# Optimization experiments

Hardware: AMD Instinct MI355X
Metric: run time of the kernel (lower is better)

## Reference

```python
import jax, jax.numpy as jnp
import numpy as np

NEG_INF = -1.0e10  # matches -10000000000.0 in the original


def setup_inputs() -> dict:
    key0 = jax.random.key(0)
    kq, kk, kv = jax.random.split(key0, 3)
    b, t, n, n_kv, d = 1, 2048, 32, 8, 128
    query = jax.random.normal(kq, (b, t, n, d), dtype=jnp.float32)
    key = jax.random.normal(kk, (b, t, n_kv, d), dtype=jnp.float32)
    value = jax.random.normal(kv, (b, t, n_kv, d), dtype=jnp.float32)
    return {"query": query, "key": key, "value": value}


def reference(query, key, value):
    """PagedAttentionOp prefill path: paged_dot_product_attention_with_max_and_sum.

    Returns (attn, local_max, local_sums) exactly as the flax module does.
    """
    b, t, n, d = query.shape
    _, s, n_kv, _ = key.shape
    g = n // n_kv  # query heads per KV head (GQA group size)
    q = jnp.reshape(query, (b, t, n_kv, g, d))
    # [b, n_kv, g, t, s]
    attn_weights = jnp.einsum("btkgd,bskd->bkgts", q, key)
    causal_mask = jnp.triu(jnp.ones((t, s), dtype=bool), k=1)[None, None, None]
    masked = jnp.where(causal_mask, NEG_INF, attn_weights)
    local_max = jnp.max(masked, axis=-1, keepdims=True)          # [b,k,g,t,1]
    local_exps = jnp.exp(masked - local_max)
    local_sums = jnp.sum(local_exps, axis=-1, keepdims=True)     # [b,k,g,t,1]
    attn = jnp.einsum("bkgts,bskd->btkgd", local_exps, value)
    attn = jnp.reshape(attn, (b, t, n, d))
    # move the t axis to position 1 then flatten (k,g) -> n
    local_max = jnp.reshape(jnp.moveaxis(local_max, -2, 1), (b, t, n, 1))
    local_sums = jnp.reshape(jnp.moveaxis(local_sums, -2, 1), (b, t, n, 1))
    return attn, local_max, local_sums
```

## Files before the change

### kernel.cpp

```cpp
#include <hip/hip_runtime.h>
#include <hip/hip_bf16.h>

#define TT  2048
#define NH  32
#define NKV 8
#define DD  128
#define KVB 64
#define THR 8.0f

typedef __attribute__((ext_vector_type(8)))  short  short8;
typedef __attribute__((ext_vector_type(4)))  float  f32x4;
typedef __attribute__((ext_vector_type(16))) float  f32x16;
typedef unsigned int u32;
typedef __attribute__((ext_vector_type(4)))  u32    u32x4;

static __device__ __forceinline__ short f2bf(float x) {
  __bf16 b = (__bf16)x;
  return __builtin_bit_cast(short, b);
}
static __device__ __forceinline__ short8 cvt8(f32x4 a, f32x4 b) {
  short8 r;
  r[0]=f2bf(a[0]); r[1]=f2bf(a[1]); r[2]=f2bf(a[2]); r[3]=f2bf(a[3]);
  r[4]=f2bf(b[0]); r[5]=f2bf(b[1]); r[6]=f2bf(b[2]); r[7]=f2bf(b[3]);
  return r;
}
static __device__ __forceinline__ u32 pk2(float lo, float hi) {
  const u32 a = (u32)(unsigned short)f2bf(lo);
  const u32 b = (u32)(unsigned short)f2bf(hi);
  return a | (b << 16);
}
static __device__ __forceinline__ void gload_lds16(const short* g, short* l) {
  __builtin_amdgcn_global_load_lds(
      (const __attribute__((address_space(1))) u32*)g,
      (__attribute__((address_space(3))) u32*)l, 16, 0, 0);
}

__global__ __launch_bounds__(256) void preconv(
    const float* __restrict__ K, const float* __restrict__ V,
    short* __restrict__ Kbf, short* __restrict__ Vtbf)
{
  const int t = threadIdx.x;
  if (blockIdx.x >= 256) {
    const int b  = blockIdx.x - 256;
    const int rr = (b << 6) + (t >> 2);
    const int q  = t & 3;
    const int j = rr >> 3, kvh = rr & 7;
    const float* src = K + (size_t)rr * DD + q * 32;
    short* dst = Kbf + ((size_t)kvh * TT + j) * DD + q * 32;
#pragma unroll
    for (int i = 0; i < 4; ++i) {
      f32x4 a  = *reinterpret_cast<const f32x4*>(src + i * 8);
      f32x4 bb = *reinterpret_cast<const f32x4*>(src + i * 8 + 4);
      *reinterpret_cast<short8*>(dst + i * 8) = cvt8(a, bb);
    }
  } else {
    const int kvh = blockIdx.x >> 5, jt = blockIdx.x & 31;
    __shared__ short Vl[64][136];
    const int jl = t >> 2, q = t & 3;
    const float* src = V + ((size_t)(jt * 64 + jl) * NKV + kvh) * DD + q * 32;
#pragma unroll
    for (int i = 0; i < 4; ++i) {
      f32x4 a  = *reinterpret_cast<const f32x4*>(src + i * 8);
      f32x4 bb = *reinterpret_cast<const f32x4*>(src + i * 8 + 4);
      *reinterpret_cast<short8*>(&Vl[jl][q * 32 + i * 8]) = cvt8(a, bb);
    }
    __syncthreads();
    const int d = t >> 1, jh = t & 1;
    short8 o[4];
#pragma unroll
    for (int k = 0; k < 4; ++k)
#pragma unroll
      for (int i = 0; i < 8; ++i)
        o[k][i] = Vl[jh * 32 + k * 8 + i][d];
    short* dst = Vtbf + ((size_t)kvh * DD + d) * TT + jt * 64 + jh * 32;
#pragma unroll
    for (int k = 0; k < 4; ++k)
      *reinterpret_cast<short8*>(dst + k * 8) = o[k];
  }
}

__global__ __launch_bounds__(512, 2) void attn_fwd(
    const float* __restrict__ Q, const short* __restrict__ Kbf,
    const short* __restrict__ Vtbf, float* __restrict__ O,
    float* __restrict__ Mo, float* __restrict__ Lo)
{
  __shared__ __align__(16) short smem[2*KVB*DD + 2*DD*KVB];
  __shared__ float sx[3][2][4][32];

  short (*Kb)[KVB][DD] = reinterpret_cast<short(*)[KVB][DD]>(&smem[0]);
  short (*Vt)[DD][KVB] = reinterpret_cast<short(*)[DD][KVB]>(&smem[2*KVB*DD]);

  const int bid  = blockIdx.x;
  const int kvh  = bid & (NKV - 1);
  const int q32  = 63 - (bid >> 3);
  const int wv   = threadIdx.x >> 6;
  const int headq= wv & 3;
  const int kh   = wv >> 2;
  const int lane = threadIdx.x & 63;
  const int l31  = lane & 31;
  const int hiK  = lane >> 5;
  const int l7   = lane & 7;
  const int head = kvh * 4 + headq;
  const int qbase = q32 * 32;
  const int q    = qbase + l31;

  const int krow0 = 8 * wv + (lane >> 4);
  const int koff0 = krow0 * DD + ((lane & 15) ^ (krow0 & 7)) * 8;
  const int krow1 = krow0 + 4;
  const int koff1 = krow1 * DD + ((lane & 15) ^ (krow1 & 7)) * 8;
  const int vrow0 = 16 * wv + (lane >> 3);
  const int voff0 = vrow0 * TT + ((lane & 7) ^ (lane >> 3)) * 8;
  const int voff1 = voff0 + 8 * TT;

  short8 aq[8];
  {
    const float* qp = Q + ((size_t)q * NH + head) * DD + hiK * 8;
#pragma unroll
    for (int ks = 0; ks < 8; ++ks) {
      const float* p = qp + ks * 16;
      aq[ks] = cvt8(*reinterpret_cast<const f32x4*>(p),
                    *reinterpret_cast<const f32x4*>(p + 4));
    }
  }

  f32x16 acc[4];
#pragma unroll
  for (int i = 0; i < 4; ++i) acc[i] = (f32x16)0.0f;
  float m = -INFINITY, tmaxh = -INFINITY, lsum = 0.0f;

  const int ntiles = (q32 >> 1) + 1;

  const short* kgp = Kbf + (size_t)kvh * TT * DD;
  const short* vgp = Vtbf + (size_t)kvh * DD * TT;

  gload_lds16(kgp + koff0, &Kb[0][8 * wv][0]);
  gload_lds16(kgp + koff1, &Kb[0][8 * wv + 4][0]);
  gload_lds16(vgp + voff0, &Vt[0][16 * wv][0]);
  gload_lds16(vgp + voff1, &Vt[0][16 * wv + 8][0]);
  kgp += (size_t)KVB * DD;
  vgp += KVB;

  for (int jt = 0; jt < ntiles; ++jt) {
    const int j0  = jt << 6;
    const int buf = jt & 1;

    __syncthreads();

    if (jt + 1 < ntiles) {
      const int nb = buf ^ 1;
      gload_lds16(kgp + koff0, &Kb[nb][8 * wv][0]);
      gload_lds16(kgp + koff1, &Kb[nb][8 * wv + 4][0]);
      gload_lds16(vgp + voff0, &Vt[nb][16 * wv][0]);
      gload_lds16(vgp + voff1, &Vt[nb][16 * wv + 8][0]);
      kgp += (size_t)KVB * DD;
      vgp += KVB;
    }

    f32x16 st = (f32x16)0.0f;
    const short* kr = &Kb[buf][kh * 32 + l31][0];
    __builtin_amdgcn_s_setprio(1);
#pragma unroll
    for (int ks = 0; ks < 8; ++ks) {
      const int c = ((ks << 1) | hiK) ^ l7;
      short8 kb = *reinterpret_cast<const short8*>(kr + c * 8);
      st = __builtin_amdgcn_mfma_f32_32x32x16_bf16(kb, aq[ks], st, 0, 0, 0);
    }
    __builtin_amdgcn_s_setprio(0);

    if (jt == ntiles - 1) {
#pragma unroll
      for (int r = 0; r < 16; ++r) {
        const int key = j0 + kh * 32 + (r & 3) + 8 * (r >> 2) + 4 * hiK;
        if (key > q) st[r] = -1.0e10f;
      }
    }

    float mx = st[0];
#pragma unroll
    for (int r = 1; r < 16; ++r) mx = fmaxf(mx, st[r]);
    mx = fmaxf(mx, __shfl_xor(mx, 32, 64));
    tmaxh = fmaxf(tmaxh, mx);

    if (__any(mx > m + THR)) {
      const float mn = fmaxf(m, mx);
      const float sc = __expf(m - mn);
      m = mn;
      lsum *= sc;
#pragma unroll
      for (int r = 0; r < 16; ++r) {
        const float sf = __shfl(sc, (r & 3) + 8 * (r >> 2) + 4 * hiK, 64);
        acc[0][r] *= sf; acc[1][r] *= sf; acc[2][r] *= sf; acc[3][r] *= sf;
      }
    }

    float e[16];
#pragma unroll
    for (int r = 0; r < 16; ++r) e[r] = __expf(st[r] - m);
    lsum += (((e[0]+e[1])+(e[2]+e[3]))+((e[4]+e[5])+(e[6]+e[7])))
          + (((e[8]+e[9])+(e[10]+e[11]))+((e[12]+e[13])+(e[14]+e[15])));

    short8 pa[2];
#pragma unroll
    for (int h2 = 0; h2 < 2; ++h2) {
      const int b = 8 * h2;
      u32 u0 = pk2(e[b+0], e[b+1]);
      u32 u1 = pk2(e[b+2], e[b+3]);
      u32 u2 = pk2(e[b+4], e[b+5]);
      u32 u3 = pk2(e[b+6], e[b+7]);
      u32 sA = hiK ? u0 : u2;
      u32 sB = hiK ? u1 : u3;
      u32 rA = __shfl_xor(sA, 32, 64);
      u32 rB = __shfl_xor(sB, 32, 64);
      u32x4 w;
      w[0] = hiK ? rA : u0;
      w[1] = hiK ? rB : u1;
      w[2] = hiK ? u2 : rA;
      w[3] = hiK ? u3 : rB;
      pa[h2] = __builtin_bit_cast(short8, w);
    }

    __builtin_amdgcn_s_setprio(1);
#pragma unroll
    for (int dg = 0; dg < 4; ++dg) {
      const short* vr = &Vt[buf][dg * 32 + l31][0];
#pragma unroll
      for (int h2 = 0; h2 < 2; ++h2) {
        const int ksv = 2 * kh + h2;
        const int c = ((ksv << 1) | hiK) ^ l7;
        short8 vb = *reinterpret_cast<const short8*>(vr + c * 8);
        acc[dg] = __builtin_amdgcn_mfma_f32_32x32x16_bf16(pa[h2], vb, acc[dg], 0, 0, 0);
      }
    }
    __builtin_amdgcn_s_setprio(0);
  }

  const float lw = lsum + __shfl_xor(lsum, 32, 64);
  __syncthreads();
  if (lane < 32) {
    sx[0][kh][headq][lane] = m;
    sx[1][kh][headq][lane] = tmaxh;
    sx[2][kh][headq][lane] = lw;
  }
  __syncthreads();
  const float mo   = sx[0][kh ^ 1][headq][l31];
  const float to   = sx[1][kh ^ 1][headq][l31];
  const float lo2  = sx[2][kh ^ 1][headq][l31];
  const float tmax = fmaxf(tmaxh, to);
  const float fsA  = __expf(m - tmax);
  const float ltot = lw * fsA + lo2 * __expf(mo - tmax);

  float* mbuf = reinterpret_cast<float*>(&smem[0]);
  if (kh == 1) {
#pragma unroll
    for (int r = 0; r < 16; ++r) {
      const int row = (r & 3) + 8 * (r >> 2) + 4 * hiK;
      const float sfr = __shfl(fsA, row, 64);
#pragma unroll
      for (int dg = 0; dg < 4; ++dg)
        mbuf[headq * 4096 + row * 128 + dg * 32 + l31] = acc[dg][r] * sfr;
    }
  }
  __syncthreads();
  if (kh == 0) {
#pragma unroll
    for (int r = 0; r < 16; ++r) {
      const int row = (r & 3) + 8 * (r >> 2) + 4 * hiK;
      const float sfr = __shfl(fsA, row, 64);
      const size_t ob = ((size_t)(qbase + row) * NH + head) * DD + l31;
#pragma unroll
      for (int dg = 0; dg < 4; ++dg)
        O[ob + dg * 32] = acc[dg][r] * sfr + mbuf[headq * 4096 + row * 128 + dg * 32 + l31];
    }
    if (lane < 32) {
      Mo[(size_t)q * NH + head] = tmax;
      Lo[(size_t)q * NH + head] = ltot;
    }
  }
}

extern "C" void kernel_launch(void* const* d_in, const int* in_sizes, int n_in,
                              void* d_out, int out_size, void* d_ws, size_t ws_size,
                              hipStream_t stream) {
  const float* Q = (const float*)d_in[0];
  const float* K = (const float*)d_in[1];
  const float* V = (const float*)d_in[2];
  float* O  = (float*)d_out;
  float* Mo = O + (size_t)TT * NH * DD;
  float* Lo = Mo + (size_t)TT * NH;
  short* Kbf  = (short*)d_ws;
  short* Vtbf = Kbf + (size_t)NKV * TT * DD;
  preconv<<<dim3(512), dim3(256), 0, stream>>>(K, V, Kbf, Vtbf);
  attn_fwd<<<dim3(64 * NKV), dim3(512), 0, stream>>>(Q, Kbf, Vtbf, O, Mo, Lo);
}
```

Before: 86.04 us.

## Double KV tile to 128 keys and issue prefetch after QK MFMAs

Raises the KV tile from 64 to 128 keys, so each iteration computes two 32-key score blocks and runs four PV MFMAs per output group. This halves loop trips and block barriers. The global-to-LDS prefetch of the next tile now starts after the QK MFMAs instead of before them, and the load swizzle is recomputed for the larger tile. In exchange, LDS use doubles, which may lower blocks per CU, and the last causal tile is coarser, so more masked keys are computed for nothing.

```diff
diff --git a/kernel.cpp b/kernel.cpp
--- a/kernel.cpp
+++ b/kernel.cpp
@@ -5,7 +5,7 @@
 #define NH  32
 #define NKV 8
 #define DD  128
-#define KVB 64
+#define KVB 128
 #define THR 8.0f
 
 typedef __attribute__((ext_vector_type(8)))  short  short8;
@@ -104,13 +104,14 @@
   const int qbase = q32 * 32;
   const int q    = qbase + l31;
 
-  const int krow0 = 8 * wv + (lane >> 4);
-  const int koff0 = krow0 * DD + ((lane & 15) ^ (krow0 & 7)) * 8;
-  const int krow1 = krow0 + 4;
-  const int koff1 = krow1 * DD + ((lane & 15) ^ (krow1 & 7)) * 8;
-  const int vrow0 = 16 * wv + (lane >> 3);
-  const int voff0 = vrow0 * TT + ((lane & 7) ^ (lane >> 3)) * 8;
-  const int voff1 = voff0 + 8 * TT;
+  int koff[4], voff[4];
+#pragma unroll
+  for (int t = 0; t < 4; ++t) {
+    const int row = 16 * wv + 4 * t + (lane >> 4);
+    const int sw  = (lane & 15) ^ (4 * (t & 1) + (lane >> 4));
+    koff[t] = row * DD + sw * 8;
+    voff[t] = row * TT + sw * 8;
+  }
 
   short8 aq[8];
   {
@@ -128,56 +129,66 @@
   for (int i = 0; i < 4; ++i) acc[i] = (f32x16)0.0f;
   float m = -INFINITY, tmaxh = -INFINITY, lsum = 0.0f;
 
-  const int ntiles = (q32 >> 1) + 1;
+  const int ntiles = (q32 + 4) >> 2;
 
   const short* kgp = Kbf + (size_t)kvh * TT * DD;
   const short* vgp = Vtbf + (size_t)kvh * DD * TT;
 
-  gload_lds16(kgp + koff0, &Kb[0][8 * wv][0]);
-  gload_lds16(kgp + koff1, &Kb[0][8 * wv + 4][0]);
-  gload_lds16(vgp + voff0, &Vt[0][16 * wv][0]);
-  gload_lds16(vgp + voff1, &Vt[0][16 * wv + 8][0]);
+#pragma unroll
+  for (int t = 0; t < 4; ++t)
+    gload_lds16(kgp + koff[t], &Kb[0][16 * wv + 4 * t][0]);
+#pragma unroll
+  for (int t = 0; t < 4; ++t)
+    gload_lds16(vgp + voff[t], &Vt[0][16 * wv + 4 * t][0]);
   kgp += (size_t)KVB * DD;
   vgp += KVB;
 
   for (int jt = 0; jt < ntiles; ++jt) {
-    const int j0  = jt << 6;
+    const int j0  = jt << 7;
     const int buf = jt & 1;
 
     __syncthreads();
+
+    f32x16 st[2];
+    st[0] = (f32x16)0.0f; st[1] = (f32x16)0.0f;
+    __builtin_amdgcn_s_setprio(1);
+#pragma unroll
+    for (int kg = 0; kg < 2; ++kg) {
+      const short* kr = &Kb[buf][kh * 64 + kg * 32 + l31][0];
+#pragma unroll
+      for (int ks = 0; ks < 8; ++ks) {
+        const int c = ((ks << 1) | hiK) ^ l7;
+        short8 kb = *reinterpret_cast<const short8*>(kr + c * 8);
+        st[kg] = __builtin_amdgcn_mfma_f32_32x32x16_bf16(kb, aq[ks], st[kg], 0, 0, 0);
+      }
+    }
+    __builtin_amdgcn_s_setprio(0);
 
     if (jt + 1 < ntiles) {
       const int nb = buf ^ 1;
-      gload_lds16(kgp + koff0, &Kb[nb][8 * wv][0]);
-      gload_lds16(kgp + koff1, &Kb[nb][8 * wv + 4][0]);
-      gload_lds16(vgp + voff0, &Vt[nb][16 * wv][0]);
-      gload_lds16(vgp + voff1, &Vt[nb][16 * wv + 8][0]);
+#pragma unroll
+      for (int t = 0; t < 4; ++t)
+        gload_lds16(kgp + koff[t], &Kb[nb][16 * wv + 4 * t][0]);
+#pragma unroll
+      for (int t = 0; t < 4; ++t)
+        gload_lds16(vgp + voff[t], &Vt[nb][16 * wv + 4 * t][0]);
       kgp += (size_t)KVB * DD;
       vgp += KVB;
     }
 
-    f32x16 st = (f32x16)0.0f;
-    const short* kr = &Kb[buf][kh * 32 + l31][0];
-    __builtin_amdgcn_s_setprio(1);
-#pragma unroll
-    for (int ks = 0; ks < 8; ++ks) {
-      const int c = ((ks << 1) | hiK) ^ l7;
-      short8 kb = *reinterpret_cast<const short8*>(kr + c * 8);
-      st = __builtin_amdgcn_mfma_f32_32x32x16_bf16(kb, aq[ks], st, 0, 0, 0);
-    }
-    __builtin_amdgcn_s_setprio(0);
-
     if (jt == ntiles - 1) {
 #pragma unroll
-      for (int r = 0; r < 16; ++r) {
-        const int key = j0 + kh * 32 + (r & 3) + 8 * (r >> 2) + 4 * hiK;
-        if (key > q) st[r] = -1.0e10f;
-      }
-    }
-
-    float mx = st[0];
-#pragma unroll
-    for (int r = 1; r < 16; ++r) mx = fmaxf(mx, st[r]);
+      for (int kg = 0; kg < 2; ++kg)
+#pragma unroll
+        for (int r = 0; r < 16; ++r) {
+          const int key = j0 + kh * 64 + kg * 32 + (r & 3) + 8 * (r >> 2) + 4 * hiK;
+          if (key > q) st[kg][r] = -1.0e10f;
+        }
+    }
+
+    float mx = fmaxf(st[0][0], st[1][0]);
+#pragma unroll
+    for (int r = 1; r < 16; ++r) mx = fmaxf(mx, fmaxf(st[0][r], st[1][r]));
     mx = fmaxf(mx, __shfl_xor(mx, 32, 64));
     tmaxh = fmaxf(tmaxh, mx);
 
@@ -193,30 +204,32 @@
       }
     }
 
-    float e[16];
-#pragma unroll
-    for (int r = 0; r < 16; ++r) e[r] = __expf(st[r] - m);
-    lsum += (((e[0]+e[1])+(e[2]+e[3]))+((e[4]+e[5])+(e[6]+e[7])))
-          + (((e[8]+e[9])+(e[10]+e[11]))+((e[12]+e[13])+(e[14]+e[15])));
-
-    short8 pa[2];
-#pragma unroll
-    for (int h2 = 0; h2 < 2; ++h2) {
-      const int b = 8 * h2;
-      u32 u0 = pk2(e[b+0], e[b+1]);
-      u32 u1 = pk2(e[b+2], e[b+3]);
-      u32 u2 = pk2(e[b+4], e[b+5]);
-      u32 u3 = pk2(e[b+6], e[b+7]);
-      u32 sA = hiK ? u0 : u2;
-      u32 sB = hiK ? u1 : u3;
-      u32 rA = __shfl_xor(sA, 32, 64);
-      u32 rB = __shfl_xor(sB, 32, 64);
-      u32x4 w;
-      w[0] = hiK ? rA : u0;
-      w[1] = hiK ? rB : u1;
-      w[2] = hiK ? u2 : rA;
-      w[3] = hiK ? u3 : rB;
-      pa[h2] = __builtin_bit_cast(short8, w);
+    short8 pa[4];
+#pragma unroll
+    for (int kg = 0; kg < 2; ++kg) {
+      float e[16];
+#pragma unroll
+      for (int r = 0; r < 16; ++r) e[r] = __expf(st[kg][r] - m);
+      lsum += (((e[0]+e[1])+(e[2]+e[3]))+((e[4]+e[5])+(e[6]+e[7])))
+            + (((e[8]+e[9])+(e[10]+e[11]))+((e[12]+e[13])+(e[14]+e[15])));
+#pragma unroll
+      for (int h2 = 0; h2 < 2; ++h2) {
+        const int b = 8 * h2;
+        u32 u0 = pk2(e[b+0], e[b+1]);
+        u32 u1 = pk2(e[b+2], e[b+3]);
+        u32 u2 = pk2(e[b+4], e[b+5]);
+        u32 u3 = pk2(e[b+6], e[b+7]);
+        u32 sA = hiK ? u0 : u2;
+        u32 sB = hiK ? u1 : u3;
+        u32 rA = __shfl_xor(sA, 32, 64);
+        u32 rB = __shfl_xor(sB, 32, 64);
+        u32x4 w4;
+        w4[0] = hiK ? rA : u0;
+        w4[1] = hiK ? rB : u1;
+        w4[2] = hiK ? u2 : rA;
+        w4[3] = hiK ? u3 : rB;
+        pa[kg * 2 + h2] = __builtin_bit_cast(short8, w4);
+      }
     }
 
     __builtin_amdgcn_s_setprio(1);
@@ -224,11 +237,10 @@
     for (int dg = 0; dg < 4; ++dg) {
       const short* vr = &Vt[buf][dg * 32 + l31][0];
 #pragma unroll
-      for (int h2 = 0; h2 < 2; ++h2) {
-        const int ksv = 2 * kh + h2;
-        const int c = ((ksv << 1) | hiK) ^ l7;
+      for (int pi = 0; pi < 4; ++pi) {
+        const int c = (8 * kh + 2 * pi + hiK) ^ l7;
         short8 vb = *reinterpret_cast<const short8*>(vr + c * 8);
-        acc[dg] = __builtin_amdgcn_mfma_f32_32x32x16_bf16(pa[h2], vb, acc[dg], 0, 0, 0);
+        acc[dg] = __builtin_amdgcn_mfma_f32_32x32x16_bf16(pa[pi], vb, acc[dg], 0, 0, 0);
       }
     }
     __builtin_amdgcn_s_setprio(0);
```

Measured after the change: 77.60 us, median of 3. -9.8%, faster.
